# Optimization experiments

Hardware: AMD Instinct MI355X
Metric: run time of the kernel (lower is better)

The kernel has to match this reference:

```python
import jax, jax.numpy as jnp
from jax import lax
import numpy as np

N = 64  # nPoints
N_ANGS = N * (N - 1) // 2

# lexicographic (top, btm) pair order used by OrthonormalMatrixGenerationSystem
_tops, _btms = np.triu_indices(N, k=1)
TOPS = jnp.asarray(_tops, dtype=jnp.int32)
BTMS = jnp.asarray(_btms, dtype=jnp.int32)


def build_R(angles, mus):
    """Sequential Givens-rotation chain: R = diag(mus) @ G_{nAngs-1} ... G_0 @ I."""
    def step(R, inp):
        ang, t, b = inp
        c, s = jnp.cos(ang), jnp.sin(ang)
        rt, rb = R[t], R[b]
        R = R.at[t].set(c * rt - s * rb).at[b].set(s * rt + c * rb)
        return R, None

    R0 = jnp.eye(N, dtype=angles.dtype)
    R, _ = lax.scan(step, R0, (angles, TOPS, BTMS))
    return mus[:, None] * R


def setup_inputs() -> dict:
    key = jax.random.key(0)
    k1, k2 = jax.random.split(key)
    X = jax.random.normal(k1, (N, 300000), dtype=jnp.float32)
    angles = jax.random.normal(k2, (N_ANGS,), dtype=jnp.float32)
    mus = jnp.ones((N,), dtype=jnp.float32)
    return {"X": X, "angles": angles, "mus": mus}


def reference(X, angles, mus):
    # mode='Analysis': Y = R @ X
    R = build_R(angles, mus)
    return R @ X
```

## Files before the change

### kernel.cpp

```cpp
#include <hip/hip_runtime.h>

#define NPTS  64
#define NANG  2016
#define NCOLS 300000
#define NC4   (NCOLS / 4)

typedef float v4 __attribute__((ext_vector_type(4)));

#define PSTR 68


__device__ __forceinline__ float rl(float x, int lane) {
    return __uint_as_float(__builtin_amdgcn_readlane(__float_as_uint(x), lane));
}

__device__ __forceinline__ float load_ang(const float* __restrict__ angles,
                                          int t, int lane) {
    int base = 63 * t - (t * (t - 1)) / 2;
    int idx  = base + lane;
    idx = idx < NANG ? idx : NANG - 1;
    return angles[idx];
}

__device__ __forceinline__ void make_cs(float a, int t, int lane,
                                        float& c, float& s) {
    const int real = 63 - t;
    const float ang = (lane < real) ? a : 0.0f;
    float sv, cv;
    sincosf(ang, &sv, &cv);
    s = sv; c = cv;
}

template<int RS>
__device__ __forceinline__ void combine_step(float* __restrict__ P,
                                             const float* __restrict__ Ms,
                                             int tid)
{
    const int c4 = tid & 15;
    const int rg = tid >> 4;
    constexpr int NR   = 64 - RS;
    constexpr int NIT  = (NR + 15) / 16;
    constexpr int K4_0 = RS / 4;

    v4 acc[NIT];
    #pragma unroll
    for (int it = 0; it < NIT; ++it) acc[it] = (v4)0.0f;

    #pragma unroll 2
    for (int k4 = K4_0; k4 < 16; ++k4) {
        v4 pv[4];
        #pragma unroll
        for (int j = 0; j < 4; ++j)
            pv[j] = *(const v4*)(P + (4 * k4 + j) * PSTR + 4 * c4);
        #pragma unroll
        for (int it = 0; it < NIT; ++it) {
            const int r = RS + rg + 16 * it;
            const v4 mv = *(const v4*)(Ms + r * PSTR + 4 * k4);
            acc[it] += pv[0] * mv.x;
            acc[it] += pv[1] * mv.y;
            acc[it] += pv[2] * mv.z;
            acc[it] += pv[3] * mv.w;
        }
    }
    __syncthreads();
    #pragma unroll
    for (int it = 0; it < NIT; ++it) {
        const int r = RS + rg + 16 * it;
        *(v4*)(P + r * PSTR + 4 * c4) = acc[it];
    }
    __syncthreads();
}

__global__ __launch_bounds__(256, 1) void ortho_build_R(
    const float* __restrict__ angles, const float* __restrict__ mus,
    float* __restrict__ AT_out)
{
    __shared__ float P[NPTS * PSTR];
    __shared__ float M[3][NPTS * PSTR];

    const int tid  = threadIdx.x;
    const int lane = tid & 63;
    const int wv   = tid >> 6;

    float* slab = (wv == 0) ? P : M[wv - 1];
    const int TA = 16 * wv;
    const int TB = (wv == 3) ? 63 : TA + 16;

    float S[64];
    #pragma unroll
    for (int j = 0; j < 64; ++j) S[j] = (TA + j == lane) ? 1.0f : 0.0f;

    float c0, s0;
    {
        const float a0 = load_ang(angles, TA, lane);
        make_cs(a0, TA, lane, c0, s0);
    }
    float a1 = load_ang(angles, TA + 1, lane);

    #pragma clang loop unroll(disable)
    for (int t = TA; t < TB; ++t) {
        const float a2 = load_ang(angles, t + 2, lane);
        float c1, s1;
        make_cs(a1, t + 1, lane, c1, s1);

        float rt = S[0];
        #pragma unroll
        for (int i = 1; i <= 63; ++i) {
            const float cc = rl(c0, i - 1);
            const float ss = rl(s0, i - 1);
            const float rb = S[i];
            S[i - 1] = fmaf(ss, rt, cc * rb);
            rt       = fmaf(cc, rt, -ss * rb);
        }
        slab[t * PSTR + lane] = rt;

        c0 = c1; s0 = s1; a1 = a2;
    }

    if (wv == 0) {
        #pragma unroll
        for (int j = 0; j < 48; ++j) slab[(16 + j) * PSTR + lane] = S[j];
    } else if (wv == 1) {
        #pragma unroll
        for (int j = 0; j < 32; ++j) slab[(32 + j) * PSTR + lane] = S[j];
    } else if (wv == 2) {
        #pragma unroll
        for (int j = 0; j < 16; ++j) slab[(48 + j) * PSTR + lane] = S[j];
    } else {
        slab[63 * PSTR + lane] = S[0];
    }
    __syncthreads();

    combine_step<16>(P, M[0], tid);
    combine_step<32>(P, M[1], tid);
    combine_step<48>(P, M[2], tid);

    #pragma unroll
    for (int i = 0; i < 16; ++i) {
        const int idx = i * 256 + tid;
        const int r   = idx & 63;
        const int k   = idx >> 6;
        AT_out[k * NPTS + r] = mus[r] * P[r * PSTR + k];
    }
}

__global__ __launch_bounds__(512) void ortho_apply(
    const float* __restrict__ X, const float* __restrict__ AT,
    float* __restrict__ Y)
{
    const int tc = threadIdx.x & 63;
    const int wv = threadIdx.x >> 6;
    const int tr = __builtin_amdgcn_readfirstlane(wv);
    const int r0 = tr * 8;

    const int j4 = blockIdx.x * 64 + tc;
    if (j4 >= NC4) return;

    const v4* xp = (const v4*)X + j4;

    v4 acc[8];
    #pragma unroll
    for (int i = 0; i < 8; ++i) acc[i] = (v4)0.0f;

    v4 xa[4], xb[4];
    #pragma unroll
    for (int q = 0; q < 4; ++q) xa[q] = xp[q * NC4];

    for (int k0 = 0; k0 < NPTS; k0 += 8) {
        #pragma unroll
        for (int q = 0; q < 4; ++q) xb[q] = xp[(k0 + 4 + q) * NC4];
        #pragma unroll
        for (int q = 0; q < 4; ++q) {
            const v4 a  = *(const v4*)(AT + (k0 + q) * NPTS + r0);
            const v4 a2 = *(const v4*)(AT + (k0 + q) * NPTS + r0 + 4);
            acc[0] += xa[q] * a.x;  acc[1] += xa[q] * a.y;
            acc[2] += xa[q] * a.z;  acc[3] += xa[q] * a.w;
            acc[4] += xa[q] * a2.x; acc[5] += xa[q] * a2.y;
            acc[6] += xa[q] * a2.z; acc[7] += xa[q] * a2.w;
        }
        #pragma unroll
        for (int q = 0; q < 4; ++q) xa[q] = xp[((k0 + 8 + q) & 63) * NC4];
        #pragma unroll
        for (int q = 0; q < 4; ++q) {
            const v4 a  = *(const v4*)(AT + (k0 + 4 + q) * NPTS + r0);
            const v4 a2 = *(const v4*)(AT + (k0 + 4 + q) * NPTS + r0 + 4);
            acc[0] += xb[q] * a.x;  acc[1] += xb[q] * a.y;
            acc[2] += xb[q] * a.z;  acc[3] += xb[q] * a.w;
            acc[4] += xb[q] * a2.x; acc[5] += xb[q] * a2.y;
            acc[6] += xb[q] * a2.z; acc[7] += xb[q] * a2.w;
        }
    }

    #pragma unroll
    for (int i = 0; i < 8; ++i) {
        v4* yp = (v4*)(Y + (size_t)(r0 + i) * NCOLS) + j4;
        __builtin_nontemporal_store(acc[i], yp);
    }
}

extern "C" void kernel_launch(void* const* d_in, const int* in_sizes, int n_in,
                              void* d_out, int out_size, void* d_ws, size_t ws_size,
                              hipStream_t stream) {
    const float* X      = (const float*)d_in[0];
    const float* angles = (const float*)d_in[1];
    const float* mus    = (const float*)d_in[2];
    float* Y  = (float*)d_out;
    float* AT = (float*)d_ws;

    ortho_build_R<<<1, 256, 0, stream>>>(angles, mus, AT);

    const int nblk = (NC4 + 63) / 64;
    ortho_apply<<<nblk, 512, 0, stream>>>(X, AT, Y);
}
```

Baseline: 176.2 us.

## Compute all 64 output rows per thread for one column in apply kernel

The apply kernel is restructured so each thread owns a single scalar column and accumulates all 64 output rows, in place of 8 waves each computing 8 rows of a float4 column. X is read exactly once per column instead of once per wave (8x redundant, though cached), and the AT loads become wave-uniform scalar loads. The cost is 64 accumulators per thread, which raises register pressure and lowers occupancy, and global accesses shrink from 16-byte vectors to 4-byte scalars. Out-of-range columns are clamped rather than returned early, so the edge threads redundantly write the last column.

Result: faster. 167.5 us (-4.9%).

```diff
diff --git a/kernel.cpp b/kernel.cpp
--- a/kernel.cpp
+++ b/kernel.cpp
@@ -144,58 +144,60 @@
     }
 }
 
-__global__ __launch_bounds__(512) void ortho_apply(
+__global__ __launch_bounds__(256) void ortho_apply(
     const float* __restrict__ X, const float* __restrict__ AT,
     float* __restrict__ Y)
 {
-    const int tc = threadIdx.x & 63;
-    const int wv = threadIdx.x >> 6;
-    const int tr = __builtin_amdgcn_readfirstlane(wv);
-    const int r0 = tr * 8;
-
-    const int j4 = blockIdx.x * 64 + tc;
-    if (j4 >= NC4) return;
-
-    const v4* xp = (const v4*)X + j4;
-
-    v4 acc[8];
-    #pragma unroll
-    for (int i = 0; i < 8; ++i) acc[i] = (v4)0.0f;
-
-    v4 xa[4], xb[4];
-    #pragma unroll
-    for (int q = 0; q < 4; ++q) xa[q] = xp[q * NC4];
+    const int lane = threadIdx.x & 63;
+    const int wv   = threadIdx.x >> 6;
+    int col = blockIdx.x * 256 + wv * 64 + lane;
+    if (col >= NCOLS) col = NCOLS - 1;
+
+    const float* xp = X + col;
+    const v4* ATv = (const v4*)AT;
+
+    float acc[64];
+    #pragma unroll
+    for (int r = 0; r < 64; ++r) acc[r] = 0.0f;
+
+    float xa[4], xb[4];
+    #pragma unroll
+    for (int q = 0; q < 4; ++q) xa[q] = xp[(size_t)q * NCOLS];
 
     for (int k0 = 0; k0 < NPTS; k0 += 8) {
         #pragma unroll
-        for (int q = 0; q < 4; ++q) xb[q] = xp[(k0 + 4 + q) * NC4];
-        #pragma unroll
-        for (int q = 0; q < 4; ++q) {
-            const v4 a  = *(const v4*)(AT + (k0 + q) * NPTS + r0);
-            const v4 a2 = *(const v4*)(AT + (k0 + q) * NPTS + r0 + 4);
-            acc[0] += xa[q] * a.x;  acc[1] += xa[q] * a.y;
-            acc[2] += xa[q] * a.z;  acc[3] += xa[q] * a.w;
-            acc[4] += xa[q] * a2.x; acc[5] += xa[q] * a2.y;
-            acc[6] += xa[q] * a2.z; acc[7] += xa[q] * a2.w;
-        }
-        #pragma unroll
-        for (int q = 0; q < 4; ++q) xa[q] = xp[((k0 + 8 + q) & 63) * NC4];
-        #pragma unroll
-        for (int q = 0; q < 4; ++q) {
-            const v4 a  = *(const v4*)(AT + (k0 + 4 + q) * NPTS + r0);
-            const v4 a2 = *(const v4*)(AT + (k0 + 4 + q) * NPTS + r0 + 4);
-            acc[0] += xb[q] * a.x;  acc[1] += xb[q] * a.y;
-            acc[2] += xb[q] * a.z;  acc[3] += xb[q] * a.w;
-            acc[4] += xb[q] * a2.x; acc[5] += xb[q] * a2.y;
-            acc[6] += xb[q] * a2.z; acc[7] += xb[q] * a2.w;
-        }
-    }
-
-    #pragma unroll
-    for (int i = 0; i < 8; ++i) {
-        v4* yp = (v4*)(Y + (size_t)(r0 + i) * NCOLS) + j4;
-        __builtin_nontemporal_store(acc[i], yp);
-    }
+        for (int q = 0; q < 4; ++q) xb[q] = xp[(size_t)(k0 + 4 + q) * NCOLS];
+        #pragma unroll
+        for (int kk = 0; kk < 4; ++kk) {
+            const int k = k0 + kk;
+            #pragma unroll
+            for (int rq = 0; rq < 16; ++rq) {
+                const v4 a = ATv[k * 16 + rq];
+                acc[4 * rq + 0] += xa[kk] * a.x;
+                acc[4 * rq + 1] += xa[kk] * a.y;
+                acc[4 * rq + 2] += xa[kk] * a.z;
+                acc[4 * rq + 3] += xa[kk] * a.w;
+            }
+        }
+        #pragma unroll
+        for (int q = 0; q < 4; ++q) xa[q] = xp[(size_t)((k0 + 8 + q) & 63) * NCOLS];
+        #pragma unroll
+        for (int kk = 0; kk < 4; ++kk) {
+            const int k = k0 + 4 + kk;
+            #pragma unroll
+            for (int rq = 0; rq < 16; ++rq) {
+                const v4 a = ATv[k * 16 + rq];
+                acc[4 * rq + 0] += xb[kk] * a.x;
+                acc[4 * rq + 1] += xb[kk] * a.y;
+                acc[4 * rq + 2] += xb[kk] * a.z;
+                acc[4 * rq + 3] += xb[kk] * a.w;
+            }
+        }
+    }
+
+    #pragma unroll
+    for (int r = 0; r < 64; ++r)
+        __builtin_nontemporal_store(acc[r], Y + (size_t)r * NCOLS + col);
 }
 
 extern "C" void kernel_launch(void* const* d_in, const int* in_sizes, int n_in,
@@ -209,6 +211,6 @@
 
     ortho_build_R<<<1, 256, 0, stream>>>(angles, mus, AT);
 
-    const int nblk = (NC4 + 63) / 64;
-    ortho_apply<<<nblk, 512, 0, stream>>>(X, AT, Y);
-}
+    const int nblk = (NCOLS + 255) / 256;
+    ortho_apply<<<nblk, 256, 0, stream>>>(X, AT, Y);
+}
```
